# Kernel optimization log

Hardware: AMD Instinct MI355X
Metric: run time of the kernel (lower is better)

## Reference

```python
import jax, jax.numpy as jnp
import numpy as np
from jax import lax

LN_EPS = 1e-5

D_MODEL, N_HEADS, HEAD_DIM, RANK, POWER_K = 1024, 16, 64, 32, 4
RIDGE_EPS, SPECTRAL_GAMMA = 1e-4, 0.99


def setup_inputs() -> dict:
    key = jax.random.key(0)
    ks = jax.random.split(key, 8)
    B, T = 4, 4096
    s = 1.0 / np.sqrt(D_MODEL)
    inp = {
        "hidden_states": jax.random.normal(ks[0], (B, T, D_MODEL), dtype=jnp.float32),
        "Wk": jax.random.normal(ks[1], (D_MODEL, N_HEADS * RANK), dtype=jnp.float32) * s,
        "Wq": jax.random.normal(ks[2], (D_MODEL, N_HEADS * RANK), dtype=jnp.float32) * s,
        "Wv": jax.random.normal(ks[3], (D_MODEL, N_HEADS * HEAD_DIM), dtype=jnp.float32) * s,
        "Wo": jax.random.normal(ks[4], (N_HEADS * HEAD_DIM, D_MODEL), dtype=jnp.float32) * s,
        "ln_scale": jnp.ones((D_MODEL,), jnp.float32),
        "ln_bias": jnp.zeros((D_MODEL,), jnp.float32),
        "gate_alpha": jnp.zeros((1,), jnp.float32),
        "log_ridge": jnp.array(np.log(RIDGE_EPS), jnp.float32),
        "log_gamma": jnp.array(np.log(SPECTRAL_GAMMA), jnp.float32),
        "prefix_len": 2048,
    }
    return inp


def _tri_solve(L, b, transpose=False):
    # solves L x = b (or L^T x = b) with lower-triangular L; batched over leading dims
    return lax.linalg.triangular_solve(L, b, left_side=True, lower=True, transpose_a=transpose)


def _build_operator(keys, values, ridge, gamma):
    # keys: (B,H,L,r), values: (B,H,L,dh)
    r = keys.shape[-1]
    G = jnp.einsum('bhlr,bhls->bhrs', keys, keys) + ridge * jnp.eye(r, dtype=keys.dtype)
    M = jnp.einsum('bhlr,bhls->bhrs', keys[:, :, 1:, :], keys[:, :, :-1, :])
    L = jnp.linalg.cholesky(G)                       # (B,H,r,r)
    U = _tri_solve(L, M)                             # L^{-1} M
    V = _tri_solve(L, jnp.swapaxes(U, -1, -2))       # L^{-1} (L^{-1}M)^T
    A_w = jnp.swapaxes(V, -1, -2)                    # L^{-1} M L^{-T}
    gamma_c = jnp.minimum(gamma, 1.0)
    sigma = jnp.linalg.svd(A_w, compute_uv=False)[..., 0]  # spectral norm
    sigma = jnp.maximum(sigma, 1e-8)
    scale = gamma_c / jnp.maximum(sigma, 1.0)
    A_w = A_w * scale[..., None, None]
    C_v = jnp.einsum('bhld,bhlr->bhdr', values, keys)       # (B,H,dh,r)
    Y = _tri_solve(L, jnp.swapaxes(C_v, -1, -2))            # L^{-1} C_v^T
    Bv_T = _tri_solve(L, Y, transpose=True)                 # G^{-1} C_v^T
    B_v = jnp.swapaxes(Bv_T, -1, -2)                        # (B,H,dh,r)
    return A_w, L, B_v


def _spectral_filter(A_w, L, B_v, queries, power_K):
    # queries: (B,H,Q,r) -> (B,H,Q,dh)
    qT = jnp.swapaxes(queries, -1, -2)      # (B,H,r,Q)
    w = _tri_solve(L, qT)                   # whiten
    for _ in range(power_K):
        w = jnp.matmul(A_w, w)
    z_hat = jnp.matmul(L, w)                # unwhiten
    out = jnp.matmul(B_v, z_hat)            # (B,H,dh,Q)
    return jnp.swapaxes(out, -1, -2)


def reference(hidden_states, Wk, Wq, Wv, Wo, ln_scale, ln_bias,
              gate_alpha, log_ridge, log_gamma, prefix_len):
    B, T, D = hidden_states.shape
    P = max(1, min(int(prefix_len), T - 1))
    mu = jnp.mean(hidden_states, axis=-1, keepdims=True)
    var = jnp.var(hidden_states, axis=-1, keepdims=True)
    normed = (hidden_states - mu) / jnp.sqrt(var + LN_EPS) * ln_scale + ln_bias
    def proj(W, dim):
        y = normed @ W
        return jnp.swapaxes(y.reshape(B, T, N_HEADS, dim), 1, 2)  # (B,H,T,dim)
    keys_all = proj(Wk, RANK)
    queries_all = proj(Wq, RANK)
    values_all = proj(Wv, HEAD_DIM)
    ridge = jnp.exp(log_ridge)
    gamma = jnp.exp(log_gamma)
    A_w, L, B_v = _build_operator(keys_all[:, :, :P, :], values_all[:, :, :P, :], ridge, gamma)
    q_out = _spectral_filter(A_w, L, B_v, queries_all[:, :, P:, :], POWER_K)
    p_out = _spectral_filter(A_w, L, B_v, keys_all[:, :, :P, :], POWER_K)
    full = jnp.concatenate([p_out, q_out], axis=2)               # (B,H,T,dh)
    full = jnp.swapaxes(full, 1, 2).reshape(B, T, N_HEADS * HEAD_DIM)
    out = full @ Wo
    return jax.nn.sigmoid(gate_alpha) * out
```

## Files before the change

### kernel.cpp

```cpp
#include <hip/hip_runtime.h>
#include <math.h>

#define D_MODEL 1024
#define TT 4096
#define NB 4
#define NH 16
#define TCH 8

typedef __attribute__((ext_vector_type(8))) short s8v;
typedef __attribute__((ext_vector_type(4))) float f4v;
typedef __attribute__((ext_vector_type(8))) unsigned short u16x8;

#define OFF_STATS ((size_t)0)
#define OFF_GP    ((size_t)(1) << 20)
#define OFF_MP    ((size_t)(3) << 20)
#define OFF_CP    ((size_t)(5) << 20)
#define OFF_FT    ((size_t)(9) << 20)
#define OFF_WKH   ((size_t)(10) << 20)
#define OFF_WKL   ((size_t)(11) << 20)
#define OFF_WQH   ((size_t)(12) << 20)
#define OFF_WQL   ((size_t)(13) << 20)
#define OFF_WVH   ((size_t)(14) << 20)
#define OFF_WVL   ((size_t)(16) << 20)
#define OFF_WOH   ((size_t)(18) << 20)
#define OFF_WOL   ((size_t)(20) << 20)
#define OFF_Y1    ((size_t)(22) << 20)
#define OFF_Y2    ((size_t)(54) << 20)
#define OFF_FH    OFF_Y2

__device__ __forceinline__ unsigned short bf16_rne(float x) {
  unsigned u = __float_as_uint(x);
  return (unsigned short)((u + 0x7fffu + ((u >> 16) & 1u)) >> 16);
}
__device__ __forceinline__ void split_bf16(float x, unsigned short& h, unsigned short& l) {
  unsigned u = __float_as_uint(x);
  unsigned r = (u + 0x7fffu + ((u >> 16) & 1u)) & 0xffff0000u;
  h = (unsigned short)(r >> 16);
  float res = x - __uint_as_float(r);
  l = bf16_rne(res);
}

__device__ __forceinline__ void gll16(unsigned short* lds, const unsigned short* g) {
  __builtin_amdgcn_global_load_lds(
      (__attribute__((address_space(1))) void*)(void*)(g),
      (__attribute__((address_space(3))) void*)(lds), 16, 0, 0);
}

__device__ __forceinline__ void xcd_swz(int gx, int gy, int& x, int& y, int& z) {
  int wg = blockIdx.x + gx * (blockIdx.y + gy * blockIdx.z);
  int k = wg & 7, j = wg >> 3;
  x = j % gx;
  int yz = k + ((j / gx) << 3);
  y = yz % gy;
  z = yz / gy;
}

__global__ __launch_bounds__(256) void ln_stats_k(const float* __restrict__ X,
                                                  float* __restrict__ stats) {
  int r = blockIdx.x;
  const float4 v = ((const float4*)(X + (size_t)r * D_MODEL))[threadIdx.x];
  float s  = v.x + v.y + v.z + v.w;
  float ss = v.x * v.x + v.y * v.y + v.z * v.z + v.w * v.w;
#pragma unroll
  for (int off = 32; off > 0; off >>= 1) {
    s  += __shfl_down(s, off, 64);
    ss += __shfl_down(ss, off, 64);
  }
  __shared__ float as_[4], bs_[4];
  int w = threadIdx.x >> 6, lane = threadIdx.x & 63;
  if (lane == 0) { as_[w] = s; bs_[w] = ss; }
  __syncthreads();
  if (threadIdx.x == 0) {
    float S  = as_[0] + as_[1] + as_[2] + as_[3];
    float SS = bs_[0] + bs_[1] + bs_[2] + bs_[3];
    float mu  = S * (1.0f / D_MODEL);
    float var = SS * (1.0f / D_MODEL) - mu * mu;
    stats[2 * (size_t)r]     = mu;
    stats[2 * (size_t)r + 1] = 1.0f / sqrtf(var + 1e-5f);
  }
}

__global__ __launch_bounds__(256) void prep_w_k(const float* __restrict__ W, int N,
                                                unsigned short* __restrict__ Thi,
                                                unsigned short* __restrict__ Tlo,
                                                int swz) {
  __shared__ float tileT[32 * 33];
  const int n0 = blockIdx.x * 32, k0 = blockIdx.y * 32;
  const int tid = threadIdx.x;
  {
    int k_l = tid >> 3, n4 = (tid & 7) << 2;
    float4 v = *(const float4*)&W[(size_t)(k0 + k_l) * N + n0 + n4];
    tileT[(n4 + 0) * 33 + k_l] = v.x;
    tileT[(n4 + 1) * 33 + k_l] = v.y;
    tileT[(n4 + 2) * 33 + k_l] = v.z;
    tileT[(n4 + 3) * 33 + k_l] = v.w;
  }
  __syncthreads();
  {
    int n_l = tid >> 3, k4 = (tid & 7) << 2;
    unsigned short h[4], l[4];
#pragma unroll
    for (int i = 0; i < 4; i++) split_bf16(tileT[n_l * 33 + k4 + i], h[i], l[i]);
    int kc = k0 + k4;
    int col = swz ? ((kc & ~63) | ((((kc >> 3) & 7) ^ (n_l & 7)) << 3) | (kc & 7)) : kc;
    *(ushort4*)&Thi[(size_t)(n0 + n_l) * 1024 + col] = make_ushort4(h[0], h[1], h[2], h[3]);
    *(ushort4*)&Tlo[(size_t)(n0 + n_l) * 1024 + col] = make_ushort4(l[0], l[1], l[2], l[3]);
  }
}

__global__ __launch_bounds__(512) void gemm_proj_k(
    const float* __restrict__ X, const float* __restrict__ stats,
    const float* __restrict__ lng, const float* __restrict__ lnb,
    const unsigned short* __restrict__ WThi, const unsigned short* __restrict__ WTlo,
    int Nw, const int* __restrict__ pref, int mode, float* __restrict__ Y) {
  int P = pref[0]; P = P < 1 ? 1 : (P > TT - 1 ? TT - 1 : P);
  int xx, yy, zz;
  xcd_swz(4, 32, xx, yy, zz);
  const int b  = zz;
  const int t0 = yy * 128;
  const int n0 = xx * 256;
  if (mode == 1) { if (t0 + 128 <= P) return; }
  else           { if (t0 >= P) return; }
  const int row0 = b * TT + t0;
  __shared__ __align__(16) unsigned short Ah[128 * 40], Al[128 * 40];
  __shared__ __align__(16) unsigned short Bh[256 * 32], Bl[256 * 32];
  __shared__ float mus[128], rss[128];
  const int tid = threadIdx.x;
  if (tid < 128) {
    mus[tid] = stats[2 * (size_t)(row0 + tid)];
    rss[tid] = stats[2 * (size_t)(row0 + tid) + 1];
  }
  const int lane = tid & 63;
  const int wid  = tid >> 6;
  const int wm = (wid >> 2) * 64, wn = (wid & 3) * 64;
  const int lm = lane & 15, lq = lane >> 4;
  const int srow = lane >> 2, scol = (lane & 3) << 3;
  f4v acc[4][4];
#pragma unroll
  for (int i = 0; i < 4; i++)
#pragma unroll
    for (int j = 0; j < 4; j++) acc[i][j] = (f4v){0.f, 0.f, 0.f, 0.f};

  for (int kt = 0; kt < D_MODEL; kt += 32) {
    __syncthreads();
#pragma unroll
    for (int s = 0; s < 2; s++) {
      int seg = wid * 2 + s;
      int brow = n0 + seg * 16 + srow;
      gll16(&Bh[seg * 512], &WThi[(size_t)brow * 1024 + kt + scol]);
      gll16(&Bl[seg * 512], &WTlo[(size_t)brow * 1024 + kt + scol]);
    }
    {
      int m = tid >> 2, k8 = (tid & 3) << 3;
      const float* src = &X[(size_t)(row0 + m) * D_MODEL + kt + k8];
      float mu = mus[m], rs = rss[m];
      u16x8 hv, lv;
#pragma unroll
      for (int i = 0; i < 8; i++) {
        float nv = (src[i] - mu) * rs * lng[kt + k8 + i] + lnb[kt + k8 + i];
        unsigned short h, l;
        split_bf16(nv, h, l);
        hv[i] = h; lv[i] = l;
      }
      *(u16x8*)&Ah[m * 40 + k8] = hv;
      *(u16x8*)&Al[m * 40 + k8] = lv;
    }
    __syncthreads();
    s8v ah[4], al[4], bh[4], bl[4];
#pragma unroll
    for (int i = 0; i < 4; i++) {
      int ar = (wm + i * 16 + lm) * 40 + lq * 8;
      int br = (wn + i * 16 + lm) * 32 + lq * 8;
      ah[i] = *(const s8v*)&Ah[ar];
      al[i] = *(const s8v*)&Al[ar];
      bh[i] = *(const s8v*)&Bh[br];
      bl[i] = *(const s8v*)&Bl[br];
    }
#pragma unroll
    for (int mi = 0; mi < 4; mi++)
#pragma unroll
      for (int ni = 0; ni < 4; ni++) {
        acc[mi][ni] = __builtin_amdgcn_mfma_f32_16x16x32_bf16(ah[mi], bh[ni], acc[mi][ni], 0, 0, 0);
        acc[mi][ni] = __builtin_amdgcn_mfma_f32_16x16x32_bf16(ah[mi], bl[ni], acc[mi][ni], 0, 0, 0);
        acc[mi][ni] = __builtin_amdgcn_mfma_f32_16x16x32_bf16(al[mi], bh[ni], acc[mi][ni], 0, 0, 0);
      }
  }
#pragma unroll
  for (int mi = 0; mi < 4; mi++) {
#pragma unroll
    for (int r = 0; r < 4; r++) {
      int t = t0 + wm + mi * 16 + lq * 4 + r;
      bool ok = (mode == 1) ? (t >= P) : (t < P);
      if (!ok) continue;
      size_t orow = (mode == 2) ? ((size_t)b * P + t) : ((size_t)b * TT + t);
#pragma unroll
      for (int ni = 0; ni < 4; ni++)
        Y[orow * Nw + n0 + wn + ni * 16 + lm] = acc[mi][ni][r];
    }
  }
}

__global__ __launch_bounds__(512) void gemm_kq_k(
    const float* __restrict__ X, const float* __restrict__ stats,
    const float* __restrict__ lng, const float* __restrict__ lnb,
    const unsigned short* __restrict__ KH, const unsigned short* __restrict__ KL,
    const unsigned short* __restrict__ QH, const unsigned short* __restrict__ QL,
    const int* __restrict__ pref, float* __restrict__ Y) {
  int P = pref[0]; P = P < 1 ? 1 : (P > TT - 1 ? TT - 1 : P);
  int xx, yy, zz;
  xcd_swz(2, 32, xx, yy, zz);
  const int b  = zz;
  const int t0 = yy * 128;
  const int n0 = xx * 256;
  const int row0 = b * TT + t0;
  const bool hasK = (t0 < P);
  const bool hasQ = (t0 + 128 > P);
  __shared__ __align__(16) unsigned short Ah[128 * 40], Al[128 * 40];
  __shared__ __align__(16) unsigned short Bh[256 * 32], Bl[256 * 32];
  __shared__ float mus[128], rss[128];
  const int tid = threadIdx.x;
  if (tid < 128) {
    mus[tid] = stats[2 * (size_t)(row0 + tid)];
    rss[tid] = stats[2 * (size_t)(row0 + tid) + 1];
  }
  const int lane = tid & 63;
  const int wid  = tid >> 6;
  const int wm = (wid >> 2) * 64, wn = (wid & 3) * 64;
  const int lm = lane & 15, lq = lane >> 4;
  const int srow = lane >> 2, scol = (lane & 3) << 3;

  for (int pass = 0; pass < 2; pass++) {
    if (pass == 0 && !hasK) continue;
    if (pass == 1 && !hasQ) continue;
    const unsigned short* WThi = pass ? QH : KH;
    const unsigned short* WTlo = pass ? QL : KL;
    f4v acc[4][4];
#pragma unroll
    for (int i = 0; i < 4; i++)
#pragma unroll
      for (int j = 0; j < 4; j++) acc[i][j] = (f4v){0.f, 0.f, 0.f, 0.f};

    for (int kt = 0; kt < D_MODEL; kt += 32) {
      __syncthreads();
#pragma unroll
      for (int s = 0; s < 2; s++) {
        int seg = wid * 2 + s;
        int brow = n0 + seg * 16 + srow;
        gll16(&Bh[seg * 512], &WThi[(size_t)brow * 1024 + kt + scol]);
        gll16(&Bl[seg * 512], &WTlo[(size_t)brow * 1024 + kt + scol]);
      }
      {
        int m = tid >> 2, k8 = (tid & 3) << 3;
        const float* src = &X[(size_t)(row0 + m) * D_MODEL + kt + k8];
        float mu = mus[m], rs = rss[m];
        u16x8 hv, lv;
#pragma unroll
        for (int i = 0; i < 8; i++) {
          float nv = (src[i] - mu) * rs * lng[kt + k8 + i] + lnb[kt + k8 + i];
          unsigned short h, l;
          split_bf16(nv, h, l);
          hv[i] = h; lv[i] = l;
        }
        *(u16x8*)&Ah[m * 40 + k8] = hv;
        *(u16x8*)&Al[m * 40 + k8] = lv;
      }
      __syncthreads();
      s8v ah[4], al[4], bh[4], bl[4];
#pragma unroll
      for (int i = 0; i < 4; i++) {
        int ar = (wm + i * 16 + lm) * 40 + lq * 8;
        int br = (wn + i * 16 + lm) * 32 + lq * 8;
        ah[i] = *(const s8v*)&Ah[ar];
        al[i] = *(const s8v*)&Al[ar];
        bh[i] = *(const s8v*)&Bh[br];
        bl[i] = *(const s8v*)&Bl[br];
      }
#pragma unroll
      for (int mi = 0; mi < 4; mi++)
#pragma unroll
        for (int ni = 0; ni < 4; ni++) {
          acc[mi][ni] = __builtin_amdgcn_mfma_f32_16x16x32_bf16(ah[mi], bh[ni], acc[mi][ni], 0, 0, 0);
          acc[mi][ni] = __builtin_amdgcn_mfma_f32_16x16x32_bf16(ah[mi], bl[ni], acc[mi][ni], 0, 0, 0);
          acc[mi][ni] = __builtin_amdgcn_mfma_f32_16x16x32_bf16(al[mi], bh[ni], acc[mi][ni], 0, 0, 0);
        }
    }
#pragma unroll
    for (int mi = 0; mi < 4; mi++) {
#pragma unroll
      for (int r = 0; r < 4; r++) {
        int t = t0 + wm + mi * 16 + lq * 4 + r;
        bool ok = pass ? (t >= P) : (t < P);
        if (!ok) continue;
#pragma unroll
        for (int ni = 0; ni < 4; ni++)
          Y[((size_t)b * TT + t) * 512 + n0 + wn + ni * 16 + lm] = acc[mi][ni][r];
      }
    }
  }
}

__global__ __launch_bounds__(256) void build_gmc_mfma_k(
    const float* __restrict__ Y1, const float* __restrict__ Y2,
    const int* __restrict__ pref,
    float* __restrict__ Gp, float* __restrict__ Mp, float* __restrict__ Cp) {
  int P = pref[0]; P = P < 1 ? 1 : (P > TT - 1 ? TT - 1 : P);
  const int c  = blockIdx.x;
  const int bh = blockIdx.y;
  const int b = bh >> 4, h = bh & 15;
  const int chunk = (P + TCH - 1) / TCH;
  const int tb = c * chunk;
  const int te = min(tb + chunk, P);

  __shared__ __align__(16) unsigned short kCh[32 * 136], kCl[32 * 136];
  __shared__ __align__(16) unsigned short kPh[32 * 136], kPl[32 * 136];
  __shared__ __align__(16) unsigned short vTh[64 * 136], vTl[64 * 136];

  const int tid = threadIdx.x;
  const int wid = tid >> 6, lane = tid & 63;
  const int lm = lane & 15, lq = lane >> 4;

  f4v acc[4];
#pragma unroll
  for (int i = 0; i < 4; i++) acc[i] = (f4v){0.f, 0.f, 0.f, 0.f};

  for (int t0 = tb; t0 < te; t0 += 128) {
    const int len = (te - t0 < 128) ? (te - t0) : 128;
    __syncthreads();
    for (int e = tid; e < 129 * 8; e += 256) {
      int row = e >> 3, j4 = (e & 7) << 2;
      int t = t0 - 1 + row;
      float4 kv = make_float4(0.f, 0.f, 0.f, 0.f);
      if (row <= len && t >= 0)
        kv = *(const float4*)&Y1[((size_t)b * TT + t) * 512 + h * 32 + j4];
      unsigned short hh[4], ll[4];
      split_bf16(kv.x, hh[0], ll[0]); split_bf16(kv.y, hh[1], ll[1]);
      split_bf16(kv.z, hh[2], ll[2]); split_bf16(kv.w, hh[3], ll[3]);
      if (row >= 1) {
#pragma unroll
        for (int q = 0; q < 4; q++) {
          kCh[(j4 + q) * 136 + row - 1] = hh[q];
          kCl[(j4 + q) * 136 + row - 1] = ll[q];
        }
      }
      if (row < 128) {
#pragma unroll
        for (int q = 0; q < 4; q++) {
          kPh[(j4 + q) * 136 + row] = hh[q];
          kPl[(j4 + q) * 136 + row] = ll[q];
        }
      }
    }
    for (int e = tid; e < 128 * 16; e += 256) {
      int row = e >> 4, dj = (e & 15) << 2;
      int t = t0 + row;
      float4 vv = make_float4(0.f, 0.f, 0.f, 0.f);
      if (row < len)
        vv = *(const float4*)&Y2[((size_t)b * P + t) * 1024 + h * 64 + dj];
      unsigned short hh[4], ll[4];
      split_bf16(vv.x, hh[0], ll[0]); split_bf16(vv.y, hh[1], ll[1]);
      split_bf16(vv.z, hh[2], ll[2]); split_bf16(vv.w, hh[3], ll[3]);
#pragma unroll
      for (int q = 0; q < 4; q++) {
        vTh[(dj + q) * 136 + row] = hh[q];
        vTl[(dj + q) * 136 + row] = ll[q];
      }
    }
    __syncthreads();

#pragma unroll
    for (int kk = 0; kk < 128; kk += 32) {
      const int off = kk + lq * 8;
      if (wid == 0) {
        s8v h0 = *(const s8v*)&kCh[(0 + lm) * 136 + off];
        s8v h1 = *(const s8v*)&kCh[(16 + lm) * 136 + off];
        s8v l0 = *(const s8v*)&kCl[(0 + lm) * 136 + off];
        s8v l1 = *(const s8v*)&kCl[(16 + lm) * 136 + off];
        acc[0] = __builtin_amdgcn_mfma_f32_16x16x32_bf16(h0, h0, acc[0], 0, 0, 0);
        acc[0] = __builtin_amdgcn_mfma_f32_16x16x32_bf16(h0, l0, acc[0], 0, 0, 0);
        acc[0] = __builtin_amdgcn_mfma_f32_16x16x32_bf16(l0, h0, acc[0], 0, 0, 0);
        acc[1] = __builtin_amdgcn_mfma_f32_16x16x32_bf16(h0, h1, acc[1], 0, 0, 0);
        acc[1] = __builtin_amdgcn_mfma_f32_16x16x32_bf16(h0, l1, acc[1], 0, 0, 0);
        acc[1] = __builtin_amdgcn_mfma_f32_16x16x32_bf16(l0, h1, acc[1], 0, 0, 0);
        acc[2] = __builtin_amdgcn_mfma_f32_16x16x32_bf16(h1, h0, acc[2], 0, 0, 0);
        acc[2] = __builtin_amdgcn_mfma_f32_16x16x32_bf16(h1, l0, acc[2], 0, 0, 0);
        acc[2] = __builtin_amdgcn_mfma_f32_16x16x32_bf16(l1, h0, acc[2], 0, 0, 0);
        acc[3] = __builtin_amdgcn_mfma_f32_16x16x32_bf16(h1, h1, acc[3], 0, 0, 0);
        acc[3] = __builtin_amdgcn_mfma_f32_16x16x32_bf16(h1, l1, acc[3], 0, 0, 0);
        acc[3] = __builtin_amdgcn_mfma_f32_16x16x32_bf16(l1, h1, acc[3], 0, 0, 0);
      } else if (wid == 1) {
        s8v ah0 = *(const s8v*)&kCh[(0 + lm) * 136 + off];
        s8v ah1 = *(const s8v*)&kCh[(16 + lm) * 136 + off];
        s8v al0 = *(const s8v*)&kCl[(0 + lm) * 136 + off];
        s8v al1 = *(const s8v*)&kCl[(16 + lm) * 136 + off];
        s8v bh0 = *(const s8v*)&kPh[(0 + lm) * 136 + off];
        s8v bh1 = *(const s8v*)&kPh[(16 + lm) * 136 + off];
        s8v bl0 = *(const s8v*)&kPl[(0 + lm) * 136 + off];
        s8v bl1 = *(const s8v*)&kPl[(16 + lm) * 136 + off];
        acc[0] = __builtin_amdgcn_mfma_f32_16x16x32_bf16(ah0, bh0, acc[0], 0, 0, 0);
        acc[0] = __builtin_amdgcn_mfma_f32_16x16x32_bf16(ah0, bl0, acc[0], 0, 0, 0);
        acc[0] = __builtin_amdgcn_mfma_f32_16x16x32_bf16(al0, bh0, acc[0], 0, 0, 0);
        acc[1] = __builtin_amdgcn_mfma_f32_16x16x32_bf16(ah0, bh1, acc[1], 0, 0, 0);
        acc[1] = __builtin_amdgcn_mfma_f32_16x16x32_bf16(ah0, bl1, acc[1], 0, 0, 0);
        acc[1] = __builtin_amdgcn_mfma_f32_16x16x32_bf16(al0, bh1, acc[1], 0, 0, 0);
        acc[2] = __builtin_amdgcn_mfma_f32_16x16x32_bf16(ah1, bh0, acc[2], 0, 0, 0);
        acc[2] = __builtin_amdgcn_mfma_f32_16x16x32_bf16(ah1, bl0, acc[2], 0, 0, 0);
        acc[2] = __builtin_amdgcn_mfma_f32_16x16x32_bf16(al1, bh0, acc[2], 0, 0, 0);
        acc[3] = __builtin_amdgcn_mfma_f32_16x16x32_bf16(ah1, bh1, acc[3], 0, 0, 0);
        acc[3] = __builtin_amdgcn_mfma_f32_16x16x32_bf16(ah1, bl1, acc[3], 0, 0, 0);
        acc[3] = __builtin_amdgcn_mfma_f32_16x16x32_bf16(al1, bh1, acc[3], 0, 0, 0);
      } else {
        const int d0 = (wid - 2) * 32;
        s8v vh0 = *(const s8v*)&vTh[(d0 + lm) * 136 + off];
        s8v vh1 = *(const s8v*)&vTh[(d0 + 16 + lm) * 136 + off];
        s8v vl0 = *(const s8v*)&vTl[(d0 + lm) * 136 + off];
        s8v vl1 = *(const s8v*)&vTl[(d0 + 16 + lm) * 136 + off];
        s8v kh0 = *(const s8v*)&kCh[(0 + lm) * 136 + off];
        s8v kh1 = *(const s8v*)&kCh[(16 + lm) * 136 + off];
        s8v kl0 = *(const s8v*)&kCl[(0 + lm) * 136 + off];
        s8v kl1 = *(const s8v*)&kCl[(16 + lm) * 136 + off];
        acc[0] = __builtin_amdgcn_mfma_f32_16x16x32_bf16(vh0, kh0, acc[0], 0, 0, 0);
        acc[0] = __builtin_amdgcn_mfma_f32_16x16x32_bf16(vh0, kl0, acc[0], 0, 0, 0);
        acc[0] = __builtin_amdgcn_mfma_f32_16x16x32_bf16(vl0, kh0, acc[0], 0, 0, 0);
        acc[1] = __builtin_amdgcn_mfma_f32_16x16x32_bf16(vh0, kh1, acc[1], 0, 0, 0);
        acc[1] = __builtin_amdgcn_mfma_f32_16x16x32_bf16(vh0, kl1, acc[1], 0, 0, 0);
        acc[1] = __builtin_amdgcn_mfma_f32_16x16x32_bf16(vl0, kh1, acc[1], 0, 0, 0);
        acc[2] = __builtin_amdgcn_mfma_f32_16x16x32_bf16(vh1, kh0, acc[2], 0, 0, 0);
        acc[2] = __builtin_amdgcn_mfma_f32_16x16x32_bf16(vh1, kl0, acc[2], 0, 0, 0);
        acc[2] = __builtin_amdgcn_mfma_f32_16x16x32_bf16(vl1, kh0, acc[2], 0, 0, 0);
        acc[3] = __builtin_amdgcn_mfma_f32_16x16x32_bf16(vh1, kh1, acc[3], 0, 0, 0);
        acc[3] = __builtin_amdgcn_mfma_f32_16x16x32_bf16(vh1, kl1, acc[3], 0, 0, 0);
        acc[3] = __builtin_amdgcn_mfma_f32_16x16x32_bf16(vl1, kh1, acc[3], 0, 0, 0);
      }
    }
  }

  if (wid < 2) {
    float* dst = (wid == 0 ? Gp : Mp) + (size_t)(c * 64 + bh) * 1024;
#pragma unroll
    for (int t = 0; t < 4; t++) {
      int i0 = (t >> 1) * 16, j0 = (t & 1) * 16;
#pragma unroll
      for (int r = 0; r < 4; r++)
        dst[(i0 + lq * 4 + r) * 32 + j0 + lm] = acc[t][r];
    }
  } else {
    float* dst = Cp + (size_t)(c * 64 + bh) * 2048;
#pragma unroll
    for (int t = 0; t < 4; t++) {
      int d0 = (wid - 2) * 32 + (t >> 1) * 16, j0 = (t & 1) * 16;
#pragma unroll
      for (int r = 0; r < 4; r++)
        dst[(d0 + lq * 4 + r) * 32 + j0 + lm] = acc[t][r];
    }
  }
}

__global__ __launch_bounds__(256) void solve_op_k(
    const float* __restrict__ Gp, const float* __restrict__ Mp,
    const float* __restrict__ Cp, const float* __restrict__ lridge,
    const float* __restrict__ lgamma, float* __restrict__ Ft) {
  __shared__ float Gs[32 * 33];
  __shared__ float Ms[32 * 32];
  __shared__ float Gi[32 * 32];
  __shared__ float W2s[32 * 33];
  __shared__ float Aw[32 * 33];
  __shared__ float Nn[32 * 32];
  __shared__ float N2[32 * 32];
  __shared__ float T1[32 * 32];
  __shared__ float Cs[64 * 32];
  __shared__ float red[256];
  const int bh = blockIdx.x;
  const int tid = threadIdx.x;
  const float ridge = expf(lridge[0]);

  for (int e = tid; e < 1024; e += 256) {
    int i = e >> 5, j = e & 31;
    float g = 0.f, m = 0.f;
#pragma unroll
    for (int cc = 0; cc < TCH; cc++) {
      g += Gp[(size_t)(cc * 64 + bh) * 1024 + e];
      m += Mp[(size_t)(cc * 64 + bh) * 1024 + e];
    }
    if (i == j) g += ridge;
    Gs[i * 33 + j] = g;
    Ms[e] = m;
  }
  for (int e = tid; e < 2048; e += 256) {
    float s = 0.f;
#pragma unroll
    for (int cc = 0; cc < TCH; cc++) s += Cp[(size_t)(cc * 64 + bh) * 2048 + e];
    Cs[e] = s;
  }
  __syncthreads();

  for (int j = 0; j < 32; j++) {
    float d = Gs[j * 33 + j];
    __syncthreads();
    float inv = 1.0f / sqrtf(d);
    if (tid >= j && tid < 32) Gs[tid * 33 + j] *= inv;
    __syncthreads();
    int w = 31 - j;
    for (int e = tid; e < w * w; e += 256) {
      int i = j + 1 + e / w, k = j + 1 + e % w;
      Gs[i * 33 + k] -= Gs[i * 33 + j] * Gs[k * 33 + j];
    }
    __syncthreads();
  }

  if (tid < 32) {
    const int c = tid;
    float w[32];
#pragma unroll
    for (int i = 0; i < 32; i++) {
      float s = (i == c) ? 1.0f : 0.0f;
#pragma unroll
      for (int j = 0; j < 32; j++)
        if (j < i) s -= Gs[i * 33 + j] * w[j];
      w[i] = s / Gs[i * 33 + i];
    }
#pragma unroll
    for (int i = 31; i >= 0; i--) {
      float s = w[i];
#pragma unroll
      for (int j = 0; j < 32; j++)
        if (j > i) s -= Gs[j * 33 + i] * w[j];
      w[i] = s / Gs[i * 33 + i];
    }
#pragma unroll
    for (int i = 0; i < 32; i++) Gi[i * 32 + c] = w[i];
  } else if (tid >= 64 && tid < 96) {
    const int c = tid - 64;
    float w[32];
#pragma unroll
    for (int i = 0; i < 32; i++) {
      float s = Ms[i * 32 + c];
#pragma unroll
      for (int j = 0; j < 32; j++)
        if (j < i) s -= Gs[i * 33 + j] * w[j];
      w[i] = s / Gs[i * 33 + i];
    }
#pragma unroll
    for (int i = 0; i < 32; i++) W2s[i * 33 + c] = w[i];
  }
  __syncthreads();
  if (tid < 32) {
    const int c = tid;
    float a[32];
#pragma unroll
    for (int i = 0; i < 32; i++) {
      float s = W2s[c * 33 + i];
#pragma unroll
      for (int j = 0; j < 32; j++)
        if (j < i) s -= Gs[i * 33 + j] * a[j];
      a[i] = s / Gs[i * 33 + i];
    }
#pragma unroll
    for (int i = 0; i < 32; i++) Aw[i * 33 + c] = a[i];
  }
  __syncthreads();

  float s0 = 0.0f;
  for (int e = tid; e < 1024; e += 256) {
    float a = Aw[(e >> 5) * 33 + (e & 31)];
    s0 += a * a;
  }
  red[tid] = s0;
  __syncthreads();
  for (int off = 128; off > 0; off >>= 1) {
    if (tid < off) red[tid] += red[tid + off];
    __syncthreads();
  }
  float frob2 = red[0];
  float sigma;
  if (frob2 <= 1.0f) {
    sigma = sqrtf(frob2);
  } else {
    if (tid < 32) {
      const int i = tid;
      float v = 1.0f + 0.001f * (float)i;
      float sig = 0.0f, prev = -1.0f;
      for (int it = 0; it < 64; it++) {
        float u = 0.0f;
#pragma unroll
        for (int j = 0; j < 32; j++) u += Aw[i * 33 + j] * __shfl(v, j, 64);
        float n2 = u * u;
#pragma unroll
        for (int o = 16; o > 0; o >>= 1) n2 += __shfl_xor(n2, o, 64);
        u /= fmaxf(sqrtf(n2), 1e-30f);
        float vn = 0.0f;
#pragma unroll
        for (int j = 0; j < 32; j++) vn += Aw[j * 33 + i] * __shfl(u, j, 64);
        float m2 = vn * vn;
#pragma unroll
        for (int o = 16; o > 0; o >>= 1) m2 += __shfl_xor(m2, o, 64);
        sig = sqrtf(m2);
        v = vn / fmaxf(sig, 1e-30f);
        if (it >= 7 && fabsf(sig - prev) <= 1e-7f * sig) break;
        prev = sig;
      }
      if (i == 0) red[0] = sig;
    }
    __syncthreads();
    sigma = red[0];
  }
  float gamma_c = fminf(expf(lgamma[0]), 1.0f);
  float scale = gamma_c / fmaxf(fmaxf(sigma, 1e-8f), 1.0f);

  for (int e = tid; e < 1024; e += 256) {
    int i = e >> 5, c = e & 31;
    float s = 0;
#pragma unroll
    for (int k = 0; k < 32; k++) s += Ms[i * 32 + k] * Gi[k * 32 + c];
    Nn[e] = scale * s;
  }
  __syncthreads();
  for (int e = tid; e < 1024; e += 256) {
    int i = e >> 5, c = e & 31;
    float s = 0;
#pragma unroll
    for (int k = 0; k < 32; k++) s += Nn[i * 32 + k] * Nn[k * 32 + c];
    N2[e] = s;
  }
  __syncthreads();
  for (int e = tid; e < 1024; e += 256) {
    int i = e >> 5, c = e & 31;
    float s = 0;
#pragma unroll
    for (int k = 0; k < 32; k++) s += N2[i * 32 + k] * N2[k * 32 + c];
    Ms[e] = s;
  }
  __syncthreads();
  for (int e = tid; e < 1024; e += 256) {
    int i = e >> 5, c = e & 31;
    float s = 0;
#pragma unroll
    for (int k = 0; k < 32; k++) s += Gi[i * 32 + k] * Ms[k * 32 + c];
    T1[e] = s;
  }
  __syncthreads();
  for (int e = tid; e < 2048; e += 256) {
    int j = e >> 6, d = e & 63;
    float s = 0;
#pragma unroll
    for (int k = 0; k < 32; k++) s += Cs[d * 32 + k] * T1[k * 32 + j];
    Ft[(size_t)bh * 2048 + e] = s;
  }
}

__global__ __launch_bounds__(256) void apply_k(const float* __restrict__ Y1,
                                               const float* __restrict__ Ft,
                                               unsigned short* __restrict__ FH) {
  __shared__ float xs[128 * 32];
  const int h = blockIdx.y;
  const int r0 = blockIdx.x * 128;
  const int bh = (r0 >> 12) * NH + h;
  const int tid = threadIdx.x;
  const int d = tid & 63, t0 = tid >> 6;
  float fcol[32];
  const float* fb = &Ft[(size_t)bh * 2048 + d];
#pragma unroll
  for (int j = 0; j < 32; j++) fcol[j] = fb[j * 64];
  for (int e = tid; e < 1024; e += 256) {
    int row = e >> 3, j4 = (e & 7) << 2;
    *(float4*)&xs[row * 32 + j4] =
        *(const float4*)&Y1[((size_t)(r0 + row)) * 512 + h * 32 + j4];
  }
  __syncthreads();
  const int dq = d >> 3, dr = d & 7;
  for (int tl = t0; tl < 128; tl += 4) {
    float s = 0;
#pragma unroll
    for (int j = 0; j < 32; j++) s += xs[tl * 32 + j] * fcol[j];
    int col = h * 64 + ((dq ^ (tl & 7)) << 3) + dr;
    FH[((size_t)(r0 + tl)) * 1024 + col] = bf16_rne(s);
  }
}

__global__ __launch_bounds__(512) void gemm_out_k(
    const unsigned short* __restrict__ FH,
    const unsigned short* __restrict__ WThi, const unsigned short* __restrict__ WTlo,
    const float* __restrict__ alpha, float* __restrict__ out) {
  __shared__ __align__(16) unsigned short lds[65536];
  int xx, yy, zz;
  xcd_swz(8, 64, xx, yy, zz);
  const int m0 = yy * 256;
  const int n0 = xx * 128;
  const int tid = threadIdx.x;
  const int lane = tid & 63;
  const int wid  = tid >> 6;
  const int wm = (wid >> 1) * 64;
  const int wn = (wid & 1) * 64;
  const int lm = lane & 15, lq = lane >> 4;
  const int l8 = lane >> 3, c8 = (lane & 7) << 3;

  f4v acc[4][4];
#pragma unroll
  for (int i = 0; i < 4; i++)
#pragma unroll
    for (int j = 0; j < 4; j++) acc[i][j] = (f4v){0.f, 0.f, 0.f, 0.f};

  auto STAGE = [&](int t, int buf) {
    const int kt = t * 64;
#pragma unroll
    for (int i = 0; i < 4; i++) {
      int iss = wid * 4 + i;
      gll16(&lds[buf * 16384 + iss * 512],
            &FH[(size_t)(m0 + iss * 8 + l8) * 1024 + kt + c8]);
    }
#pragma unroll
    for (int i = 0; i < 2; i++) {
      int iss = wid * 2 + i;
      gll16(&lds[32768 + buf * 8192 + iss * 512],
            &WThi[(size_t)(n0 + iss * 8 + l8) * 1024 + kt + c8]);
    }
#pragma unroll
    for (int i = 0; i < 2; i++) {
      int iss = wid * 2 + i;
      gll16(&lds[49152 + buf * 8192 + iss * 512],
            &WTlo[(size_t)(n0 + iss * 8 + l8) * 1024 + kt + c8]);
    }
  };

  STAGE(0, 0);
  STAGE(1, 1);

  for (int t = 0; t < 16; t++) {
    const int buf = t & 1;
    if (t < 15) asm volatile("s_waitcnt vmcnt(8)" ::: "memory");
    else        asm volatile("s_waitcnt vmcnt(0)" ::: "memory");
    __builtin_amdgcn_s_barrier();
    const unsigned short* Ab  = &lds[buf * 16384];
    const unsigned short* Bhb = &lds[32768 + buf * 8192];
    const unsigned short* Blb = &lds[49152 + buf * 8192];
    __builtin_amdgcn_s_setprio(1);
#pragma unroll
    for (int kk = 0; kk < 2; kk++) {
      s8v ah[4], bh[4], bl[4];
#pragma unroll
      for (int i = 0; i < 4; i++) {
        int rA = wm + i * 16 + lm;
        int rB = wn + i * 16 + lm;
        int sA = (((kk * 4 + lq) ^ (rA & 7)) << 3);
        int sB = (((kk * 4 + lq) ^ (rB & 7)) << 3);
        ah[i] = *(const s8v*)&Ab[rA * 64 + sA];
        bh[i] = *(const s8v*)&Bhb[rB * 64 + sB];
        bl[i] = *(const s8v*)&Blb[rB * 64 + sB];
      }
#pragma unroll
      for (int mi = 0; mi < 4; mi++)
#pragma unroll
        for (int ni = 0; ni < 4; ni++) {
          acc[mi][ni] = __builtin_amdgcn_mfma_f32_16x16x32_bf16(ah[mi], bh[ni], acc[mi][ni], 0, 0, 0);
          acc[mi][ni] = __builtin_amdgcn_mfma_f32_16x16x32_bf16(ah[mi], bl[ni], acc[mi][ni], 0, 0, 0);
        }
    }
    __builtin_amdgcn_s_setprio(0);
    __builtin_amdgcn_sched_barrier(0);
    __builtin_amdgcn_s_barrier();
    if (t < 14) STAGE(t + 2, buf);
  }

  float sg = 1.0f / (1.0f + expf(-alpha[0]));
#pragma unroll
  for (int mi = 0; mi < 4; mi++)
#pragma unroll
    for (int r = 0; r < 4; r++) {
      size_t orow = (size_t)(m0 + wm + mi * 16 + lq * 4 + r);
#pragma unroll
      for (int ni = 0; ni < 4; ni++)
        out[orow * 1024 + n0 + wn + ni * 16 + lm] = sg * acc[mi][ni][r];
    }
}

extern "C" void kernel_launch(void* const* d_in, const int* in_sizes, int n_in,
                              void* d_out, int out_size, void* d_ws, size_t ws_size,
                              hipStream_t stream) {
  const float* X      = (const float*)d_in[0];
  const float* Wk     = (const float*)d_in[1];
  const float* Wq     = (const float*)d_in[2];
  const float* Wv     = (const float*)d_in[3];
  const float* Wo     = (const float*)d_in[4];
  const float* lng    = (const float*)d_in[5];
  const float* lnb    = (const float*)d_in[6];
  const float* alpha  = (const float*)d_in[7];
  const float* lridge = (const float*)d_in[8];
  const float* lgamma = (const float*)d_in[9];
  const int*   pref   = (const int*)d_in[10];
  float* out = (float*)d_out;
  char* ws = (char*)d_ws;
  float* stats = (float*)(ws + OFF_STATS);
  float* Gp    = (float*)(ws + OFF_GP);
  float* Mp    = (float*)(ws + OFF_MP);
  float* Cp    = (float*)(ws + OFF_CP);
  float* Ft    = (float*)(ws + OFF_FT);
  unsigned short* WKH = (unsigned short*)(ws + OFF_WKH);
  unsigned short* WKL = (unsigned short*)(ws + OFF_WKL);
  unsigned short* WQH = (unsigned short*)(ws + OFF_WQH);
  unsigned short* WQL = (unsigned short*)(ws + OFF_WQL);
  unsigned short* WVH = (unsigned short*)(ws + OFF_WVH);
  unsigned short* WVL = (unsigned short*)(ws + OFF_WVL);
  unsigned short* WOH = (unsigned short*)(ws + OFF_WOH);
  unsigned short* WOL = (unsigned short*)(ws + OFF_WOL);
  float* Y1 = (float*)(ws + OFF_Y1);
  float* Y2 = (float*)(ws + OFF_Y2);
  unsigned short* FH = (unsigned short*)(ws + OFF_FH);

  ln_stats_k<<<16384, 256, 0, stream>>>(X, stats);
  prep_w_k<<<dim3(16, 32), 256, 0, stream>>>(Wk, 512, WKH, WKL, 0);
  prep_w_k<<<dim3(16, 32), 256, 0, stream>>>(Wq, 512, WQH, WQL, 0);
  prep_w_k<<<dim3(32, 32), 256, 0, stream>>>(Wv, 1024, WVH, WVL, 0);
  prep_w_k<<<dim3(32, 32), 256, 0, stream>>>(Wo, 1024, WOH, WOL, 1);
  gemm_kq_k<<<dim3(2, 32, NB), 512, 0, stream>>>(X, stats, lng, lnb, WKH, WKL, WQH, WQL, pref, Y1);
  gemm_proj_k<<<dim3(4, 32, NB), 512, 0, stream>>>(X, stats, lng, lnb, WVH, WVL, 1024, pref, 2, Y2);
  build_gmc_mfma_k<<<dim3(TCH, 64), 256, 0, stream>>>(Y1, Y2, pref, Gp, Mp, Cp);
  solve_op_k<<<64, 256, 0, stream>>>(Gp, Mp, Cp, lridge, lgamma, Ft);
  apply_k<<<dim3(128, NH), 256, 0, stream>>>(Y1, Ft, FH);
  gemm_out_k<<<dim3(8, 64), 512, 0, stream>>>(FH, WOH, WOL, alpha, out);
}
```

Baseline: 437.7 us.

## Merge LN-fused projection GEMMs into one double-buffered pipelined kernel with swizzled B

Replaces the two LayerNorm-fused projection GEMM kernels with a single kernel that double-buffers the A and B shared-memory tiles. It prefetches X and weight tiles two k-steps ahead using vmcnt waits, and caches the LN scale and bias in shared memory. The weight layout gets a new 32-column XOR swizzle so B-fragment reads avoid LDS bank conflicts, and MFMA sections raise wave priority. This aims to hide global-load latency behind the MFMAs, at the cost of doubled LDS use, which may lower occupancy. The hand-counted waitcnt values are fragile.

```diff
diff --git a/kernel.cpp b/kernel.cpp
--- a/kernel.cpp
+++ b/kernel.cpp
@@ -102,179 +102,118 @@
 #pragma unroll
     for (int i = 0; i < 4; i++) split_bf16(tileT[n_l * 33 + k4 + i], h[i], l[i]);
     int kc = k0 + k4;
-    int col = swz ? ((kc & ~63) | ((((kc >> 3) & 7) ^ (n_l & 7)) << 3) | (kc & 7)) : kc;
+    int col = kc;
+    if (swz == 1)
+      col = (kc & ~63) | ((((kc >> 3) & 7) ^ (n_l & 7)) << 3) | (kc & 7);
+    else if (swz == 2)
+      col = (kc & ~31) | ((((kc >> 3) & 3) ^ ((n_l >> 1) & 3)) << 3) | (kc & 7);
     *(ushort4*)&Thi[(size_t)(n0 + n_l) * 1024 + col] = make_ushort4(h[0], h[1], h[2], h[3]);
     *(ushort4*)&Tlo[(size_t)(n0 + n_l) * 1024 + col] = make_ushort4(l[0], l[1], l[2], l[3]);
   }
 }
 
-__global__ __launch_bounds__(512) void gemm_proj_k(
+__global__ __launch_bounds__(512) void gemm_ln_k(
     const float* __restrict__ X, const float* __restrict__ stats,
     const float* __restrict__ lng, const float* __restrict__ lnb,
-    const unsigned short* __restrict__ WThi, const unsigned short* __restrict__ WTlo,
-    int Nw, const int* __restrict__ pref, int mode, float* __restrict__ Y) {
+    const unsigned short* __restrict__ BH0, const unsigned short* __restrict__ BL0,
+    const unsigned short* __restrict__ BH1, const unsigned short* __restrict__ BL1,
+    const int* __restrict__ pref, int mode, int Nw, float* __restrict__ Y) {
   int P = pref[0]; P = P < 1 ? 1 : (P > TT - 1 ? TT - 1 : P);
   int xx, yy, zz;
-  xcd_swz(4, 32, xx, yy, zz);
+  xcd_swz(gridDim.x, 32, xx, yy, zz);
   const int b  = zz;
   const int t0 = yy * 128;
   const int n0 = xx * 256;
-  if (mode == 1) { if (t0 + 128 <= P) return; }
-  else           { if (t0 >= P) return; }
+  if (mode == 2 && t0 >= P) return;
   const int row0 = b * TT + t0;
-  __shared__ __align__(16) unsigned short Ah[128 * 40], Al[128 * 40];
-  __shared__ __align__(16) unsigned short Bh[256 * 32], Bl[256 * 32];
-  __shared__ float mus[128], rss[128];
+  const bool hasK = (t0 < P);
+  const bool hasQ = (t0 + 128 > P);
+
+  __shared__ __align__(16) unsigned short aH[2 * 128 * 40], aL[2 * 128 * 40];
+  __shared__ __align__(16) unsigned short bH[2 * 256 * 32], bL[2 * 256 * 32];
+  __shared__ float lngs[1024], lnbs[1024];
+
   const int tid = threadIdx.x;
-  if (tid < 128) {
-    mus[tid] = stats[2 * (size_t)(row0 + tid)];
-    rss[tid] = stats[2 * (size_t)(row0 + tid) + 1];
-  }
   const int lane = tid & 63;
   const int wid  = tid >> 6;
   const int wm = (wid >> 2) * 64, wn = (wid & 3) * 64;
   const int lm = lane & 15, lq = lane >> 4;
-  const int srow = lane >> 2, scol = (lane & 3) << 3;
-  f4v acc[4][4];
-#pragma unroll
-  for (int i = 0; i < 4; i++)
-#pragma unroll
-    for (int j = 0; j < 4; j++) acc[i][j] = (f4v){0.f, 0.f, 0.f, 0.f};
-
-  for (int kt = 0; kt < D_MODEL; kt += 32) {
-    __syncthreads();
-#pragma unroll
-    for (int s = 0; s < 2; s++) {
-      int seg = wid * 2 + s;
-      int brow = n0 + seg * 16 + srow;
-      gll16(&Bh[seg * 512], &WThi[(size_t)brow * 1024 + kt + scol]);
-      gll16(&Bl[seg * 512], &WTlo[(size_t)brow * 1024 + kt + scol]);
-    }
-    {
-      int m = tid >> 2, k8 = (tid & 3) << 3;
-      const float* src = &X[(size_t)(row0 + m) * D_MODEL + kt + k8];
-      float mu = mus[m], rs = rss[m];
+  const int arow = tid >> 2, acol = (tid & 3) << 3;
+  const int l4 = lane >> 2, c4 = (lane & 3) << 3;
+
+  for (int e = tid; e < 1024; e += 512) { lngs[e] = lng[e]; lnbs[e] = lnb[e]; }
+  const float mu = stats[2 * (size_t)(row0 + arow)];
+  const float rs = stats[2 * (size_t)(row0 + arow) + 1];
+
+  for (int pass = 0; pass < 2; ++pass) {
+    if (mode == 2) { if (pass == 1) break; }
+    else { if (pass == 0 && !hasK) continue; if (pass == 1 && !hasQ) continue; }
+    const unsigned short* WH = pass ? BH1 : BH0;
+    const unsigned short* WL = pass ? BL1 : BL0;
+
+    f4v acc[4][4];
+#pragma unroll
+    for (int i = 0; i < 4; i++)
+#pragma unroll
+      for (int j = 0; j < 4; j++) acc[i][j] = (f4v){0.f, 0.f, 0.f, 0.f};
+
+    float4 xE[2], xO[2];
+
+    auto XLOAD = [&](int t, float4 (&xr)[2]) {
+      const float* src = &X[(size_t)(row0 + arow) * 1024 + t * 32 + acol];
+      xr[0] = *(const float4*)src;
+      xr[1] = *(const float4*)(src + 4);
+    };
+    auto STAGEB = [&](int t, int buf) {
+      const int kt = t * 32;
+#pragma unroll
+      for (int i = 0; i < 2; i++) {
+        int iss = wid * 2 + i;
+        int r = n0 + iss * 16 + l4;
+        gll16(&bH[buf * 8192 + iss * 512], &WH[(size_t)r * 1024 + kt + c4]);
+        gll16(&bL[buf * 8192 + iss * 512], &WL[(size_t)r * 1024 + kt + c4]);
+      }
+    };
+    auto LNW = [&](int tt, float4 (&xr)[2], int abuf) {
+      const int kt = tt * 32;
+      float4 lg0 = *(const float4*)&lngs[kt + acol];
+      float4 lg1 = *(const float4*)&lngs[kt + acol + 4];
+      float4 lb0 = *(const float4*)&lnbs[kt + acol];
+      float4 lb1 = *(const float4*)&lnbs[kt + acol + 4];
+      float xv[8] = {xr[0].x, xr[0].y, xr[0].z, xr[0].w,
+                     xr[1].x, xr[1].y, xr[1].z, xr[1].w};
+      float lgv[8] = {lg0.x, lg0.y, lg0.z, lg0.w, lg1.x, lg1.y, lg1.z, lg1.w};
+      float lbv[8] = {lb0.x, lb0.y, lb0.z, lb0.w, lb1.x, lb1.y, lb1.z, lb1.w};
       u16x8 hv, lv;
 #pragma unroll
       for (int i = 0; i < 8; i++) {
-        float nv = (src[i] - mu) * rs * lng[kt + k8 + i] + lnb[kt + k8 + i];
+        float nv = (xv[i] - mu) * rs * lgv[i] + lbv[i];
         unsigned short h, l;
         split_bf16(nv, h, l);
         hv[i] = h; lv[i] = l;
       }
-      *(u16x8*)&Ah[m * 40 + k8] = hv;
-      *(u16x8*)&Al[m * 40 + k8] = lv;
-    }
-    __syncthreads();
-    s8v ah[4], al[4], bh[4], bl[4];
-#pragma unroll
-    for (int i = 0; i < 4; i++) {
-      int ar = (wm + i * 16 + lm) * 40 + lq * 8;
-      int br = (wn + i * 16 + lm) * 32 + lq * 8;
-      ah[i] = *(const s8v*)&Ah[ar];
-      al[i] = *(const s8v*)&Al[ar];
-      bh[i] = *(const s8v*)&Bh[br];
-      bl[i] = *(const s8v*)&Bl[br];
-    }
-#pragma unroll
-    for (int mi = 0; mi < 4; mi++)
-#pragma unroll
-      for (int ni = 0; ni < 4; ni++) {
-        acc[mi][ni] = __builtin_amdgcn_mfma_f32_16x16x32_bf16(ah[mi], bh[ni], acc[mi][ni], 0, 0, 0);
-        acc[mi][ni] = __builtin_amdgcn_mfma_f32_16x16x32_bf16(ah[mi], bl[ni], acc[mi][ni], 0, 0, 0);
-        acc[mi][ni] = __builtin_amdgcn_mfma_f32_16x16x32_bf16(al[mi], bh[ni], acc[mi][ni], 0, 0, 0);
-      }
-  }
-#pragma unroll
-  for (int mi = 0; mi < 4; mi++) {
-#pragma unroll
-    for (int r = 0; r < 4; r++) {
-      int t = t0 + wm + mi * 16 + lq * 4 + r;
-      bool ok = (mode == 1) ? (t >= P) : (t < P);
-      if (!ok) continue;
-      size_t orow = (mode == 2) ? ((size_t)b * P + t) : ((size_t)b * TT + t);
-#pragma unroll
-      for (int ni = 0; ni < 4; ni++)
-        Y[orow * Nw + n0 + wn + ni * 16 + lm] = acc[mi][ni][r];
-    }
-  }
-}
-
-__global__ __launch_bounds__(512) void gemm_kq_k(
-    const float* __restrict__ X, const float* __restrict__ stats,
-    const float* __restrict__ lng, const float* __restrict__ lnb,
-    const unsigned short* __restrict__ KH, const unsigned short* __restrict__ KL,
-    const unsigned short* __restrict__ QH, const unsigned short* __restrict__ QL,
-    const int* __restrict__ pref, float* __restrict__ Y) {
-  int P = pref[0]; P = P < 1 ? 1 : (P > TT - 1 ? TT - 1 : P);
-  int xx, yy, zz;
-  xcd_swz(2, 32, xx, yy, zz);
-  const int b  = zz;
-  const int t0 = yy * 128;
-  const int n0 = xx * 256;
-  const int row0 = b * TT + t0;
-  const bool hasK = (t0 < P);
-  const bool hasQ = (t0 + 128 > P);
-  __shared__ __align__(16) unsigned short Ah[128 * 40], Al[128 * 40];
-  __shared__ __align__(16) unsigned short Bh[256 * 32], Bl[256 * 32];
-  __shared__ float mus[128], rss[128];
-  const int tid = threadIdx.x;
-  if (tid < 128) {
-    mus[tid] = stats[2 * (size_t)(row0 + tid)];
-    rss[tid] = stats[2 * (size_t)(row0 + tid) + 1];
-  }
-  const int lane = tid & 63;
-  const int wid  = tid >> 6;
-  const int wm = (wid >> 2) * 64, wn = (wid & 3) * 64;
-  const int lm = lane & 15, lq = lane >> 4;
-  const int srow = lane >> 2, scol = (lane & 3) << 3;
-
-  for (int pass = 0; pass < 2; pass++) {
-    if (pass == 0 && !hasK) continue;
-    if (pass == 1 && !hasQ) continue;
-    const unsigned short* WThi = pass ? QH : KH;
-    const unsigned short* WTlo = pass ? QL : KL;
-    f4v acc[4][4];
-#pragma unroll
-    for (int i = 0; i < 4; i++)
-#pragma unroll
-      for (int j = 0; j < 4; j++) acc[i][j] = (f4v){0.f, 0.f, 0.f, 0.f};
-
-    for (int kt = 0; kt < D_MODEL; kt += 32) {
-      __syncthreads();
-#pragma unroll
-      for (int s = 0; s < 2; s++) {
-        int seg = wid * 2 + s;
-        int brow = n0 + seg * 16 + srow;
-        gll16(&Bh[seg * 512], &WThi[(size_t)brow * 1024 + kt + scol]);
-        gll16(&Bl[seg * 512], &WTlo[(size_t)brow * 1024 + kt + scol]);
-      }
-      {
-        int m = tid >> 2, k8 = (tid & 3) << 3;
-        const float* src = &X[(size_t)(row0 + m) * D_MODEL + kt + k8];
-        float mu = mus[m], rs = rss[m];
-        u16x8 hv, lv;
-#pragma unroll
-        for (int i = 0; i < 8; i++) {
-          float nv = (src[i] - mu) * rs * lng[kt + k8 + i] + lnb[kt + k8 + i];
-          unsigned short h, l;
-          split_bf16(nv, h, l);
-          hv[i] = h; lv[i] = l;
-        }
-        *(u16x8*)&Ah[m * 40 + k8] = hv;
-        *(u16x8*)&Al[m * 40 + k8] = lv;
-      }
-      __syncthreads();
+      int ao = abuf * 5120 + arow * 40 + acol;
+      *(u16x8*)&aH[ao] = hv;
+      *(u16x8*)&aL[ao] = lv;
+    };
+
+    auto ITER = [&](int t, float4 (&xrd)[2], float4 (&xwr)[2]) {
+      const int buf = t & 1;
+      asm volatile("s_waitcnt vmcnt(6)" ::: "memory");
+      __builtin_amdgcn_s_barrier();
       s8v ah[4], al[4], bh[4], bl[4];
 #pragma unroll
       for (int i = 0; i < 4; i++) {
-        int ar = (wm + i * 16 + lm) * 40 + lq * 8;
-        int br = (wn + i * 16 + lm) * 32 + lq * 8;
-        ah[i] = *(const s8v*)&Ah[ar];
-        al[i] = *(const s8v*)&Al[ar];
-        bh[i] = *(const s8v*)&Bh[br];
-        bl[i] = *(const s8v*)&Bl[br];
-      }
+        int rA = wm + i * 16 + lm;
+        int rB = wn + i * 16 + lm;
+        int ao = buf * 5120 + rA * 40 + lq * 8;
+        int bo = buf * 8192 + rB * 32 + ((lq ^ ((rB >> 1) & 3)) << 3);
+        ah[i] = *(const s8v*)&aH[ao];
+        al[i] = *(const s8v*)&aL[ao];
+        bh[i] = *(const s8v*)&bH[bo];
+        bl[i] = *(const s8v*)&bL[bo];
+      }
+      __builtin_amdgcn_s_setprio(1);
 #pragma unroll
       for (int mi = 0; mi < 4; mi++)
 #pragma unroll
@@ -283,17 +222,38 @@
           acc[mi][ni] = __builtin_amdgcn_mfma_f32_16x16x32_bf16(ah[mi], bl[ni], acc[mi][ni], 0, 0, 0);
           acc[mi][ni] = __builtin_amdgcn_mfma_f32_16x16x32_bf16(al[mi], bh[ni], acc[mi][ni], 0, 0, 0);
         }
-    }
+      __builtin_amdgcn_s_setprio(0);
+      if (t < 31) LNW(t + 1, xrd, buf ^ 1);
+      asm volatile("s_waitcnt lgkmcnt(0)" ::: "memory");
+      __builtin_amdgcn_s_barrier();
+      if (t < 30) {
+        XLOAD(t + 2, xwr);
+        STAGEB(t + 2, buf);
+      }
+    };
+
+    XLOAD(0, xE); STAGEB(0, 0);
+    XLOAD(1, xO); STAGEB(1, 1);
+    __syncthreads();
+    LNW(0, xE, 0);
+    __syncthreads();
+
+    for (int t2 = 0; t2 < 32; t2 += 2) {
+      ITER(t2,     xO, xE);
+      ITER(t2 + 1, xE, xO);
+    }
+
 #pragma unroll
     for (int mi = 0; mi < 4; mi++) {
 #pragma unroll
       for (int r = 0; r < 4; r++) {
         int t = t0 + wm + mi * 16 + lq * 4 + r;
-        bool ok = pass ? (t >= P) : (t < P);
+        bool ok = (mode == 2) ? (t < P) : (pass ? (t >= P) : (t < P));
         if (!ok) continue;
+        size_t orow = (mode == 2) ? ((size_t)b * P + t) : ((size_t)b * TT + t);
 #pragma unroll
         for (int ni = 0; ni < 4; ni++)
-          Y[((size_t)b * TT + t) * 512 + n0 + wn + ni * 16 + lm] = acc[mi][ni][r];
+          Y[orow * Nw + n0 + wn + ni * 16 + lm] = acc[mi][ni][r];
       }
     }
   }
@@ -806,12 +766,14 @@
   unsigned short* FH = (unsigned short*)(ws + OFF_FH);
 
   ln_stats_k<<<16384, 256, 0, stream>>>(X, stats);
-  prep_w_k<<<dim3(16, 32), 256, 0, stream>>>(Wk, 512, WKH, WKL, 0);
-  prep_w_k<<<dim3(16, 32), 256, 0, stream>>>(Wq, 512, WQH, WQL, 0);
-  prep_w_k<<<dim3(32, 32), 256, 0, stream>>>(Wv, 1024, WVH, WVL, 0);
+  prep_w_k<<<dim3(16, 32), 256, 0, stream>>>(Wk, 512, WKH, WKL, 2);
+  prep_w_k<<<dim3(16, 32), 256, 0, stream>>>(Wq, 512, WQH, WQL, 2);
+  prep_w_k<<<dim3(32, 32), 256, 0, stream>>>(Wv, 1024, WVH, WVL, 2);
   prep_w_k<<<dim3(32, 32), 256, 0, stream>>>(Wo, 1024, WOH, WOL, 1);
-  gemm_kq_k<<<dim3(2, 32, NB), 512, 0, stream>>>(X, stats, lng, lnb, WKH, WKL, WQH, WQL, pref, Y1);
-  gemm_proj_k<<<dim3(4, 32, NB), 512, 0, stream>>>(X, stats, lng, lnb, WVH, WVL, 1024, pref, 2, Y2);
+  gemm_ln_k<<<dim3(2, 32, NB), 512, 0, stream>>>(X, stats, lng, lnb,
+      WKH, WKL, WQH, WQL, pref, 0, 512, Y1);
+  gemm_ln_k<<<dim3(4, 32, NB), 512, 0, stream>>>(X, stats, lng, lnb,
+      WVH, WVL, WVH, WVL, pref, 2, 1024, Y2);
   build_gmc_mfma_k<<<dim3(TCH, 64), 256, 0, stream>>>(Y1, Y2, pref, Gp, Mp, Cp);
   solve_op_k<<<64, 256, 0, stream>>>(Gp, Mp, Cp, lridge, lgamma, Ft);
   apply_k<<<dim3(128, NH), 256, 0, stream>>>(Y1, Ft, FH);
```

After: 418.9 us. 1.04x faster.
